# Kernel tuning notes

Hardware: AMD Instinct MI355X
Metric: run time of the kernel (lower is better)

Reference implementation:

```python
import jax, jax.numpy as jnp
import numpy as np

B, N, FIN, FOUT, OPD = 2048, 64, 96, 128, 48
EPS = 1e-5      # nn.LayerNorm default eps
SLOPE = 0.01    # F.leaky_relu default negative_slope (used in GAT forward)


def setup_inputs() -> dict:
    key = jax.random.key(0)
    ks = jax.random.split(key, 12)
    stdv = 1.0 / np.sqrt(FOUT)
    h = jax.random.normal(ks[0], (B, N, FIN), jnp.float32)
    # binary DAG-style adjacency (float mask, as used multiplicatively in torch)
    adj = (jax.random.uniform(ks[1], (B, N, N)) < 0.3).astype(jnp.float32)
    op_emb = jax.random.normal(ks[2], (B, N, OPD), jnp.float32)
    # DenseGraphFlow params (uniform(-stdv, stdv) per reset_parameters)
    W = jax.random.uniform(ks[3], (FIN, FOUT), jnp.float32, -stdv, stdv)
    b = jax.random.uniform(ks[4], (FOUT,), jnp.float32, -stdv, stdv)
    Wop_d = jax.random.normal(ks[5], (OPD, FOUT), jnp.float32) * 0.05
    bop_d = jnp.zeros((FOUT,), jnp.float32)
    # GraphAttentionLayer params
    Wk = jax.random.normal(ks[6], (FIN, FOUT), jnp.float32) * 0.05
    a_w = jax.random.normal(ks[7], (FOUT,), jnp.float32) * 0.05
    Wop_g = jax.random.normal(ks[8], (OPD, FOUT), jnp.float32) * 0.05
    bop_g = jnp.zeros((FOUT,), jnp.float32)
    gamma = jnp.ones((FOUT,), jnp.float32)
    beta = jnp.zeros((FOUT,), jnp.float32)
    return dict(h=h, adj=adj, op_emb=op_emb, W=W, b=b, Wop_d=Wop_d, bop_d=bop_d,
                Wk=Wk, a_w=a_w, Wop_g=Wop_g, bop_g=bop_g, gamma=gamma, beta=beta)


def reference(h, adj, op_emb, W, b, Wop_d, bop_d, Wk, a_w, Wop_g, bop_g, gamma, beta):
    # ---- DenseGraphFlow (residual=True, opattention=True) ----
    support = jnp.einsum('bnf,fo->bno', h, W)                       # [B,N,FOUT]
    gate_d = jax.nn.sigmoid(op_emb @ Wop_d + bop_d)                 # [B,N,FOUT]
    dense = gate_d * jnp.einsum('bij,bjo->bio', adj, support) + support + b

    # ---- GraphAttentionLayer (unique_attn_proj=False -> Wq=Wv=Wk) ----
    Whk = jnp.einsum('bnf,fo->bno', h, Wk)                          # [B,N,FOUT]
    # torch builds a_input[b,i,j,m] = Whk[b,j,m] * Whk[b,i,m], then projects with
    # a (Linear FOUT->1). Exactly equivalent factored form (no [B,N,N,F] tensor):
    scores = jnp.einsum('bim,bjm->bij', Whk * a_w, Whk)             # [B,N,N]
    alpha = jnp.where(scores >= 0, scores, SLOPE * scores) * adj    # leaky_relu then adj mask
    attn = jax.nn.softmax(alpha, axis=-1)                           # softmax over j (torch dim=-2 of [b,i,j,1])
    hp = jnp.einsum('bij,bjo->bio', attn, Whk)                      # aggregate values
    gate_g = jax.nn.sigmoid(op_emb @ Wop_g + bop_g)
    hp = gate_g * hp
    # LayerNorm over last dim
    mu = jnp.mean(hp, axis=-1, keepdims=True)
    var = jnp.var(hp, axis=-1, keepdims=True)
    hp = (hp - mu) / jnp.sqrt(var + EPS) * gamma + beta

    # ---- ensemble combine ----
    return (dense + hp) / 2
```

## Files before the change

### kernel.cpp

```cpp
#include <hip/hip_runtime.h>

#define NB 2048
#define NN 64
#define KFIN 96
#define KFOUT 128
#define KOPD 48

typedef __attribute__((ext_vector_type(8))) short bf8;
typedef __attribute__((ext_vector_type(4))) float f32x4;
typedef __attribute__((ext_vector_type(4))) unsigned short us4;
typedef __attribute__((ext_vector_type(2))) __bf16 bfx2;

__device__ __forceinline__ unsigned short f2bf(float f) {
  __bf16 h = (__bf16)f;
  return __builtin_bit_cast(unsigned short, h);
}
__device__ __forceinline__ float bf2f(unsigned short s) {
  unsigned int u = ((unsigned int)s) << 16;
  return __builtin_bit_cast(float, u);
}
__device__ __forceinline__ us4 pack4(float a, float b, float c, float d) {
  us4 q; q.x = f2bf(a); q.y = f2bf(b); q.z = f2bf(c); q.w = f2bf(d); return q;
}
__device__ __forceinline__ bf8 pk8(float4 a, float4 b) {
  bf8 r;
  r[0] = (short)f2bf(a.x); r[1] = (short)f2bf(a.y); r[2] = (short)f2bf(a.z); r[3] = (short)f2bf(a.w);
  r[4] = (short)f2bf(b.x); r[5] = (short)f2bf(b.y); r[6] = (short)f2bf(b.z); r[7] = (short)f2bf(b.w);
  return r;
}
__device__ __forceinline__ unsigned int pk2(float lo, float hi) {
  bfx2 v; v[0] = (__bf16)lo; v[1] = (__bf16)hi;
  return __builtin_bit_cast(unsigned int, v);
}
__device__ __forceinline__ float unpk(unsigned int p, int hi) {
  return bf2f((unsigned short)(hi ? (p >> 16) : (p & 0xffffu)));
}
__device__ __forceinline__ float sigm(float x) {
  return __builtin_amdgcn_rcpf(1.f + __expf(-x));
}

__global__ void prep_weights(const float* __restrict__ W, const float* __restrict__ Wk,
                             const float* __restrict__ Wd, const float* __restrict__ Wg,
                             unsigned short* __restrict__ ws) {
  int idx = blockIdx.x * 256 + threadIdx.x;
  if (idx >= 40960) return;
  float v;
  if (idx < 24576) {
    int r  = (idx < 12288) ? idx : idx - 12288;
    const float* M = (idx < 12288) ? W : Wk;
    int nb = r / 1536, rem = r % 1536;
    int kb = rem / 512, rem2 = rem % 512;
    int l = rem2 >> 3, e = rem2 & 7;
    int o = nb * 16 + (l & 15);
    int k = kb * 32 + (l >> 4) * 8 + e;
    v = M[k * 128 + o];
  } else {
    int r  = (idx < 32768) ? idx - 24576 : idx - 32768;
    const float* M = (idx < 32768) ? Wd : Wg;
    int nb = r / 1024, rem = r % 1024;
    int kb = rem / 512, rem2 = rem % 512;
    int l = rem2 >> 3, e = rem2 & 7;
    int o = nb * 16 + (l & 15);
    int k = kb * 32 + (l >> 4) * 8 + e;
    v = (k < 48) ? M[k * 128 + o] : 0.f;
  }
  ws[idx] = f2bf(v);
}

#define LD1 68
#define LD2 132
#define LDA 68
__global__ __launch_bounds__(256, 5) void gin_fused(
    const float* __restrict__ hg, const float* __restrict__ adjg,
    const float* __restrict__ opeg, const float* __restrict__ bvec,
    const float* __restrict__ bopd, const float* __restrict__ bopg,
    const float* __restrict__ awv, const float* __restrict__ gmv,
    const float* __restrict__ btv, const unsigned short* __restrict__ ws,
    float* __restrict__ out) {
  __shared__ __align__(16) char smem[26112];
  unsigned short* buf1   = (unsigned short*)smem;
  unsigned short* attn_s = (unsigned short*)(smem + 17408);

  const int t  = threadIdx.x;
  const int b  = blockIdx.x;
  const int w  = t >> 6;
  const int l  = t & 63;
  const int lr = l & 15;
  const int lg = l >> 4;
  const int kcol = 8 * lg;
  const int arow = w * 16 + lr;
  const int rowb = w * 16 + lg * 4;

  const float* hrow = hg   + (size_t)b * (NN * KFIN) + arow * KFIN;
  const float* orow = opeg + (size_t)b * (NN * KOPD) + arow * KOPD;
  float* outp = out + (size_t)b * (NN * KFOUT);

  const unsigned short* WT  = ws;
  const unsigned short* WkT = ws + 12288;
  const unsigned short* WdT = ws + 24576;
  const unsigned short* WgT = ws + 32768;
  f32x4 zz = {0.f, 0.f, 0.f, 0.f};

  bf8 oa[2], ha[3];
  {
    float4 p0 = *(const float4*)(orow + kcol);
    float4 p1 = *(const float4*)(orow + kcol + 4);
    oa[0] = pk8(p0, p1);
    if (lg < 2) {
      float4 q0 = *(const float4*)(orow + 32 + kcol);
      float4 q1 = *(const float4*)(orow + 32 + kcol + 4);
      oa[1] = pk8(q0, q1);
    } else {
      bf8 z = {0, 0, 0, 0, 0, 0, 0, 0};
      oa[1] = z;
    }
  }
  #pragma unroll
  for (int kb = 0; kb < 3; ++kb) {
    float4 p0 = *(const float4*)(hrow + kb * 32 + kcol);
    float4 p1 = *(const float4*)(hrow + kb * 32 + kcol + 4);
    ha[kb] = pk8(p0, p1);
  }

  unsigned int gdp[8][2];
  {
    f32x4 gd[8] = {zz, zz, zz, zz, zz, zz, zz, zz};
    #pragma unroll
    for (int kb = 0; kb < 2; ++kb) {
      #pragma unroll
      for (int nb = 0; nb < 8; ++nb) {
        bf8 bb = *(const bf8*)(WdT + (nb * 2 + kb) * 512 + l * 8);
        gd[nb] = __builtin_amdgcn_mfma_f32_16x16x32_bf16(oa[kb], bb, gd[nb], 0, 0, 0);
      }
    }
    #pragma unroll
    for (int nb = 0; nb < 8; ++nb) {
      float bo = bopd[nb * 16 + lr];
      gdp[nb][0] = pk2(sigm(gd[nb][0] + bo), sigm(gd[nb][1] + bo));
      gdp[nb][1] = pk2(sigm(gd[nb][2] + bo), sigm(gd[nb][3] + bo));
    }
  }

  f32x4 sacc[8] = {zz, zz, zz, zz, zz, zz, zz, zz};
  #pragma unroll
  for (int kb = 0; kb < 3; ++kb) {
    #pragma unroll
    for (int nb = 0; nb < 8; ++nb) {
      bf8 bb = *(const bf8*)(WT + (nb * 3 + kb) * 512 + l * 8);
      sacc[nb] = __builtin_amdgcn_mfma_f32_16x16x32_bf16(ha[kb], bb, sacc[nb], 0, 0, 0);
    }
  }
  #pragma unroll
  for (int nb = 0; nb < 8; ++nb)
    *(us4*)(buf1 + (nb * 16 + lr) * LD1 + w * 16 + lg * 4) =
        pack4(sacc[nb][0], sacc[nb][1], sacc[nb][2], sacc[nb][3]);
  __syncthreads();

  unsigned int dnp[8][2];
  {
    const float* ajr = adjg + (size_t)b * (NN * NN) + arow * NN;
    bf8 aa[2];
    #pragma unroll
    for (int kb = 0; kb < 2; ++kb) {
      float4 p0 = *(const float4*)(ajr + kb * 32 + kcol);
      float4 p1 = *(const float4*)(ajr + kb * 32 + kcol + 4);
      aa[kb] = pk8(p0, p1);
    }
    #pragma unroll
    for (int nb = 0; nb < 8; ++nb) {
      f32x4 dacc = zz;
      #pragma unroll
      for (int kb = 0; kb < 2; ++kb) {
        bf8 bb = *(const bf8*)(buf1 + (nb * 16 + lr) * LD1 + kb * 32 + kcol);
        dacc = __builtin_amdgcn_mfma_f32_16x16x32_bf16(aa[kb], bb, dacc, 0, 0, 0);
      }
      float bc = bvec[nb * 16 + lr];
      float d0 = unpk(gdp[nb][0], 0) * dacc[0] + sacc[nb][0] + bc;
      float d1 = unpk(gdp[nb][0], 1) * dacc[1] + sacc[nb][1] + bc;
      float d2 = unpk(gdp[nb][1], 0) * dacc[2] + sacc[nb][2] + bc;
      float d3 = unpk(gdp[nb][1], 1) * dacc[3] + sacc[nb][3] + bc;
      dnp[nb][0] = pk2(d0, d1); dnp[nb][1] = pk2(d2, d3);
    }
  }

  f32x4 wacc[8] = {zz, zz, zz, zz, zz, zz, zz, zz};
  #pragma unroll
  for (int kb = 0; kb < 3; ++kb) {
    #pragma unroll
    for (int nb = 0; nb < 8; ++nb) {
      bf8 bb = *(const bf8*)(WkT + (nb * 3 + kb) * 512 + l * 8);
      wacc[nb] = __builtin_amdgcn_mfma_f32_16x16x32_bf16(ha[kb], bb, wacc[nb], 0, 0, 0);
    }
  }
  __syncthreads();

  #pragma unroll
  for (int nb = 0; nb < 8; ++nb) {
    int o = nb * 16 + lr;
    #pragma unroll
    for (int r = 0; r < 4; ++r)
      buf1[(w * 16 + lg * 4 + r) * LD2 + o] = f2bf(wacc[nb][r]);
  }

  unsigned int ggp[8][2];
  {
    f32x4 gg[8] = {zz, zz, zz, zz, zz, zz, zz, zz};
    #pragma unroll
    for (int kb = 0; kb < 2; ++kb) {
      #pragma unroll
      for (int nb = 0; nb < 8; ++nb) {
        bf8 bb = *(const bf8*)(WgT + (nb * 2 + kb) * 512 + l * 8);
        gg[nb] = __builtin_amdgcn_mfma_f32_16x16x32_bf16(oa[kb], bb, gg[nb], 0, 0, 0);
      }
    }
    #pragma unroll
    for (int nb = 0; nb < 8; ++nb) {
      float bo = bopg[nb * 16 + lr];
      ggp[nb][0] = pk2(sigm(gg[nb][0] + bo), sigm(gg[nb][1] + bo));
      ggp[nb][1] = pk2(sigm(gg[nb][2] + bo), sigm(gg[nb][3] + bo));
    }
  }

  float msk[4][4];
  #pragma unroll
  for (int jb = 0; jb < 4; ++jb)
    #pragma unroll
    for (int r = 0; r < 4; ++r)
      msk[jb][r] = adjg[(size_t)b * (NN * NN) + (rowb + r) * NN + jb * 16 + lr];

  __syncthreads();

  f32x4 sc[4] = {zz, zz, zz, zz};
  #pragma unroll
  for (int kb = 0; kb < 4; ++kb) {
    bf8 ar = *(const bf8*)(buf1 + arow * LD2 + kb * 32 + kcol);
    const float4* ap = (const float4*)(awv + kb * 32 + kcol);
    float4 a0 = ap[0], a1 = ap[1];
    bf8 a;
    a[0] = (short)f2bf(bf2f((unsigned short)ar[0]) * a0.x);
    a[1] = (short)f2bf(bf2f((unsigned short)ar[1]) * a0.y);
    a[2] = (short)f2bf(bf2f((unsigned short)ar[2]) * a0.z);
    a[3] = (short)f2bf(bf2f((unsigned short)ar[3]) * a0.w);
    a[4] = (short)f2bf(bf2f((unsigned short)ar[4]) * a1.x);
    a[5] = (short)f2bf(bf2f((unsigned short)ar[5]) * a1.y);
    a[6] = (short)f2bf(bf2f((unsigned short)ar[6]) * a1.z);
    a[7] = (short)f2bf(bf2f((unsigned short)ar[7]) * a1.w);
    #pragma unroll
    for (int jb = 0; jb < 4; ++jb) {
      bf8 bb = *(const bf8*)(buf1 + (jb * 16 + lr) * LD2 + kb * 32 + kcol);
      sc[jb] = __builtin_amdgcn_mfma_f32_16x16x32_bf16(a, bb, sc[jb], 0, 0, 0);
    }
  }

  float al[4][4];
  #pragma unroll
  for (int jb = 0; jb < 4; ++jb)
    #pragma unroll
    for (int r = 0; r < 4; ++r) {
      float s = sc[jb][r];
      al[jb][r] = (s >= 0.f ? s : 0.01f * s) * msk[jb][r];
    }
  #pragma unroll
  for (int r = 0; r < 4; ++r) {
    float m = fmaxf(fmaxf(al[0][r], al[1][r]), fmaxf(al[2][r], al[3][r]));
    m = fmaxf(m, __shfl_xor(m, 1));
    m = fmaxf(m, __shfl_xor(m, 2));
    m = fmaxf(m, __shfl_xor(m, 4));
    m = fmaxf(m, __shfl_xor(m, 8));
    float s0 = 0.f;
    #pragma unroll
    for (int jb = 0; jb < 4; ++jb) { float p = __expf(al[jb][r] - m); al[jb][r] = p; s0 += p; }
    s0 += __shfl_xor(s0, 1);
    s0 += __shfl_xor(s0, 2);
    s0 += __shfl_xor(s0, 4);
    s0 += __shfl_xor(s0, 8);
    float inv = __builtin_amdgcn_rcpf(s0);
    #pragma unroll
    for (int jb = 0; jb < 4; ++jb) al[jb][r] *= inv;
  }

  #pragma unroll
  for (int jb = 0; jb < 4; ++jb)
    #pragma unroll
    for (int r = 0; r < 4; ++r)
      attn_s[(rowb + r) * LDA + jb * 16 + lr] = f2bf(al[jb][r]);

  f32x4 hpacc[8] = {zz, zz, zz, zz, zz, zz, zz, zz};
  #pragma unroll
  for (int kb = 0; kb < 2; ++kb) {
    bf8 a = *(const bf8*)(attn_s + arow * LDA + kb * 32 + kcol);
    #pragma unroll
    for (int nb = 0; nb < 8; ++nb) {
      const unsigned short* gp = buf1 + (kb * 32 + 8 * lg) * LD2 + nb * 16 + lr;
      bf8 bb;
      #pragma unroll
      for (int e = 0; e < 8; ++e) bb[e] = (short)gp[e * LD2];
      hpacc[nb] = __builtin_amdgcn_mfma_f32_16x16x32_bf16(a, bb, hpacc[nb], 0, 0, 0);
    }
  }

  float gam[8], bet[8];
  #pragma unroll
  for (int nb = 0; nb < 8; ++nb) { gam[nb] = gmv[nb * 16 + lr]; bet[nb] = btv[nb * 16 + lr]; }
  #pragma unroll
  for (int r = 0; r < 4; ++r) {
    float hv[8]; float su = 0.f, sq = 0.f;
    #pragma unroll
    for (int nb = 0; nb < 8; ++nb) {
      float v = unpk(ggp[nb][r >> 1], r & 1) * hpacc[nb][r];
      hv[nb] = v; su += v; sq += v * v;
    }
    su += __shfl_xor(su, 1); su += __shfl_xor(su, 2);
    su += __shfl_xor(su, 4); su += __shfl_xor(su, 8);
    sq += __shfl_xor(sq, 1); sq += __shfl_xor(sq, 2);
    sq += __shfl_xor(sq, 4); sq += __shfl_xor(sq, 8);
    float mean = su * (1.f / 128.f);
    float var  = sq * (1.f / 128.f) - mean * mean;
    float rinv = rsqrtf(var + 1e-5f);
    int row = rowb + r;
    #pragma unroll
    for (int nb = 0; nb < 8; ++nb) {
      float hn = (hv[nb] - mean) * rinv * gam[nb] + bet[nb];
      float dv = unpk(dnp[nb][r >> 1], r & 1);
      outp[row * 128 + nb * 16 + lr] = (dv + hn) * 0.5f;
    }
  }
}

extern "C" void kernel_launch(void* const* d_in, const int* in_sizes, int n_in,
                              void* d_out, int out_size, void* d_ws, size_t ws_size,
                              hipStream_t stream) {
  const float* h     = (const float*)d_in[0];
  const float* adj   = (const float*)d_in[1];
  const float* ope   = (const float*)d_in[2];
  const float* W     = (const float*)d_in[3];
  const float* bvec  = (const float*)d_in[4];
  const float* Wopd  = (const float*)d_in[5];
  const float* bopd  = (const float*)d_in[6];
  const float* Wk    = (const float*)d_in[7];
  const float* a_w   = (const float*)d_in[8];
  const float* Wopg  = (const float*)d_in[9];
  const float* bopg  = (const float*)d_in[10];
  const float* gamma = (const float*)d_in[11];
  const float* beta  = (const float*)d_in[12];
  float* out = (float*)d_out;
  unsigned short* ws = (unsigned short*)d_ws;

  prep_weights<<<dim3(160), dim3(256), 0, stream>>>(W, Wk, Wopd, Wopg, ws);
  gin_fused<<<dim3(NB), dim3(256), 0, stream>>>(h, adj, ope, bvec, bopd, bopg,
                                                a_w, gamma, beta, ws, out);
}
```

Baseline: 121.4 us.

## Split output columns across two waves per row block with cross-wave LayerNorm

Moves to 512 threads per block, with each pair of waves sharing a 16-row block and each wave computing half of the 128 output columns. This halves per-thread accumulator registers and adds parallelism per graph. A small shared buffer exchanges LayerNorm partial sums between the paired waves, which adds one extra barrier. Support values are now kept bf16-packed, and the attention buffer becomes per-wave with a new padding. The score and softmax work is now duplicated across the two waves of each pair.

```diff
diff --git a/kernel.cpp b/kernel.cpp
--- a/kernel.cpp
+++ b/kernel.cpp
@@ -69,27 +69,31 @@
 
 #define LD1 68
 #define LD2 132
-#define LDA 68
-__global__ __launch_bounds__(256, 5) void gin_fused(
+#define LDA 72
+__global__ __launch_bounds__(512, 6) void gin_fused(
     const float* __restrict__ hg, const float* __restrict__ adjg,
     const float* __restrict__ opeg, const float* __restrict__ bvec,
     const float* __restrict__ bopd, const float* __restrict__ bopg,
     const float* __restrict__ awv, const float* __restrict__ gmv,
     const float* __restrict__ btv, const unsigned short* __restrict__ ws,
     float* __restrict__ out) {
-  __shared__ __align__(16) char smem[26112];
-  unsigned short* buf1   = (unsigned short*)smem;
-  unsigned short* attn_s = (unsigned short*)(smem + 17408);
-
-  const int t  = threadIdx.x;
-  const int b  = blockIdx.x;
-  const int w  = t >> 6;
-  const int l  = t & 63;
-  const int lr = l & 15;
-  const int lg = l >> 4;
+  __shared__ __align__(16) char smem[36864];
+  unsigned short* buf1  = (unsigned short*)smem;
+  unsigned short* attnb = (unsigned short*)(smem + 17408);
+  float2*         lnbuf = (float2*)(smem + 35840);
+
+  const int t    = threadIdx.x;
+  const int b    = blockIdx.x;
+  const int wave = t >> 6;
+  const int wr   = wave >> 1;
+  const int wc   = wave & 1;
+  const int l    = t & 63;
+  const int lr   = l & 15;
+  const int lg   = l >> 4;
   const int kcol = 8 * lg;
-  const int arow = w * 16 + lr;
-  const int rowb = w * 16 + lg * 4;
+  const int arow = wr * 16 + lr;
+  const int rowb = wr * 16 + lg * 4;
+  const int cb   = wc * 64;
 
   const float* hrow = hg   + (size_t)b * (NN * KFIN) + arow * KFIN;
   const float* orow = opeg + (size_t)b * (NN * KOPD) + arow * KOPD;
@@ -122,41 +126,47 @@
     ha[kb] = pk8(p0, p1);
   }
 
-  unsigned int gdp[8][2];
-  {
-    f32x4 gd[8] = {zz, zz, zz, zz, zz, zz, zz, zz};
+  unsigned int gdp[4][2];
+  {
+    f32x4 gd[4] = {zz, zz, zz, zz};
     #pragma unroll
     for (int kb = 0; kb < 2; ++kb) {
       #pragma unroll
-      for (int nb = 0; nb < 8; ++nb) {
-        bf8 bb = *(const bf8*)(WdT + (nb * 2 + kb) * 512 + l * 8);
+      for (int nb = 0; nb < 4; ++nb) {
+        bf8 bb = *(const bf8*)(WdT + ((wc * 4 + nb) * 2 + kb) * 512 + l * 8);
         gd[nb] = __builtin_amdgcn_mfma_f32_16x16x32_bf16(oa[kb], bb, gd[nb], 0, 0, 0);
       }
     }
     #pragma unroll
-    for (int nb = 0; nb < 8; ++nb) {
-      float bo = bopd[nb * 16 + lr];
+    for (int nb = 0; nb < 4; ++nb) {
+      float bo = bopd[cb + nb * 16 + lr];
       gdp[nb][0] = pk2(sigm(gd[nb][0] + bo), sigm(gd[nb][1] + bo));
       gdp[nb][1] = pk2(sigm(gd[nb][2] + bo), sigm(gd[nb][3] + bo));
     }
   }
 
-  f32x4 sacc[8] = {zz, zz, zz, zz, zz, zz, zz, zz};
-  #pragma unroll
-  for (int kb = 0; kb < 3; ++kb) {
-    #pragma unroll
-    for (int nb = 0; nb < 8; ++nb) {
-      bf8 bb = *(const bf8*)(WT + (nb * 3 + kb) * 512 + l * 8);
-      sacc[nb] = __builtin_amdgcn_mfma_f32_16x16x32_bf16(ha[kb], bb, sacc[nb], 0, 0, 0);
-    }
-  }
-  #pragma unroll
-  for (int nb = 0; nb < 8; ++nb)
-    *(us4*)(buf1 + (nb * 16 + lr) * LD1 + w * 16 + lg * 4) =
-        pack4(sacc[nb][0], sacc[nb][1], sacc[nb][2], sacc[nb][3]);
+  unsigned int sap[4][2];
+  {
+    f32x4 sacc[4] = {zz, zz, zz, zz};
+    #pragma unroll
+    for (int kb = 0; kb < 3; ++kb) {
+      #pragma unroll
+      for (int nb = 0; nb < 4; ++nb) {
+        bf8 bb = *(const bf8*)(WT + ((wc * 4 + nb) * 3 + kb) * 512 + l * 8);
+        sacc[nb] = __builtin_amdgcn_mfma_f32_16x16x32_bf16(ha[kb], bb, sacc[nb], 0, 0, 0);
+      }
+    }
+    #pragma unroll
+    for (int nb = 0; nb < 4; ++nb) {
+      *(us4*)(buf1 + (cb + nb * 16 + lr) * LD1 + wr * 16 + lg * 4) =
+          pack4(sacc[nb][0], sacc[nb][1], sacc[nb][2], sacc[nb][3]);
+      sap[nb][0] = pk2(sacc[nb][0], sacc[nb][1]);
+      sap[nb][1] = pk2(sacc[nb][2], sacc[nb][3]);
+    }
+  }
   __syncthreads();
 
-  unsigned int dnp[8][2];
+  unsigned int dnp[4][2];
   {
     const float* ajr = adjg + (size_t)b * (NN * NN) + arow * NN;
     bf8 aa[2];
@@ -167,55 +177,55 @@
       aa[kb] = pk8(p0, p1);
     }
     #pragma unroll
-    for (int nb = 0; nb < 8; ++nb) {
+    for (int nb = 0; nb < 4; ++nb) {
       f32x4 dacc = zz;
       #pragma unroll
       for (int kb = 0; kb < 2; ++kb) {
-        bf8 bb = *(const bf8*)(buf1 + (nb * 16 + lr) * LD1 + kb * 32 + kcol);
+        bf8 bb = *(const bf8*)(buf1 + (cb + nb * 16 + lr) * LD1 + kb * 32 + kcol);
         dacc = __builtin_amdgcn_mfma_f32_16x16x32_bf16(aa[kb], bb, dacc, 0, 0, 0);
       }
-      float bc = bvec[nb * 16 + lr];
-      float d0 = unpk(gdp[nb][0], 0) * dacc[0] + sacc[nb][0] + bc;
-      float d1 = unpk(gdp[nb][0], 1) * dacc[1] + sacc[nb][1] + bc;
-      float d2 = unpk(gdp[nb][1], 0) * dacc[2] + sacc[nb][2] + bc;
-      float d3 = unpk(gdp[nb][1], 1) * dacc[3] + sacc[nb][3] + bc;
+      float bc = bvec[cb + nb * 16 + lr];
+      float d0 = unpk(gdp[nb][0], 0) * dacc[0] + unpk(sap[nb][0], 0) + bc;
+      float d1 = unpk(gdp[nb][0], 1) * dacc[1] + unpk(sap[nb][0], 1) + bc;
+      float d2 = unpk(gdp[nb][1], 0) * dacc[2] + unpk(sap[nb][1], 0) + bc;
+      float d3 = unpk(gdp[nb][1], 1) * dacc[3] + unpk(sap[nb][1], 1) + bc;
       dnp[nb][0] = pk2(d0, d1); dnp[nb][1] = pk2(d2, d3);
     }
   }
 
-  f32x4 wacc[8] = {zz, zz, zz, zz, zz, zz, zz, zz};
+  f32x4 wacc[4] = {zz, zz, zz, zz};
   #pragma unroll
   for (int kb = 0; kb < 3; ++kb) {
     #pragma unroll
-    for (int nb = 0; nb < 8; ++nb) {
-      bf8 bb = *(const bf8*)(WkT + (nb * 3 + kb) * 512 + l * 8);
+    for (int nb = 0; nb < 4; ++nb) {
+      bf8 bb = *(const bf8*)(WkT + ((wc * 4 + nb) * 3 + kb) * 512 + l * 8);
       wacc[nb] = __builtin_amdgcn_mfma_f32_16x16x32_bf16(ha[kb], bb, wacc[nb], 0, 0, 0);
     }
   }
   __syncthreads();
 
   #pragma unroll
-  for (int nb = 0; nb < 8; ++nb) {
-    int o = nb * 16 + lr;
+  for (int nb = 0; nb < 4; ++nb) {
+    int o = cb + nb * 16 + lr;
     #pragma unroll
     for (int r = 0; r < 4; ++r)
-      buf1[(w * 16 + lg * 4 + r) * LD2 + o] = f2bf(wacc[nb][r]);
-  }
-
-  unsigned int ggp[8][2];
-  {
-    f32x4 gg[8] = {zz, zz, zz, zz, zz, zz, zz, zz};
+      buf1[(wr * 16 + lg * 4 + r) * LD2 + o] = f2bf(wacc[nb][r]);
+  }
+
+  unsigned int ggp[4][2];
+  {
+    f32x4 gg[4] = {zz, zz, zz, zz};
     #pragma unroll
     for (int kb = 0; kb < 2; ++kb) {
       #pragma unroll
-      for (int nb = 0; nb < 8; ++nb) {
-        bf8 bb = *(const bf8*)(WgT + (nb * 2 + kb) * 512 + l * 8);
+      for (int nb = 0; nb < 4; ++nb) {
+        bf8 bb = *(const bf8*)(WgT + ((wc * 4 + nb) * 2 + kb) * 512 + l * 8);
         gg[nb] = __builtin_amdgcn_mfma_f32_16x16x32_bf16(oa[kb], bb, gg[nb], 0, 0, 0);
       }
     }
     #pragma unroll
-    for (int nb = 0; nb < 8; ++nb) {
-      float bo = bopg[nb * 16 + lr];
+    for (int nb = 0; nb < 4; ++nb) {
+      float bo = bopg[cb + nb * 16 + lr];
       ggp[nb][0] = pk2(sigm(gg[nb][0] + bo), sigm(gg[nb][1] + bo));
       ggp[nb][1] = pk2(sigm(gg[nb][2] + bo), sigm(gg[nb][3] + bo));
     }
@@ -279,19 +289,20 @@
     for (int jb = 0; jb < 4; ++jb) al[jb][r] *= inv;
   }
 
+  unsigned short* attnw = attnb + wave * (16 * LDA);
   #pragma unroll
   for (int jb = 0; jb < 4; ++jb)
     #pragma unroll
     for (int r = 0; r < 4; ++r)
-      attn_s[(rowb + r) * LDA + jb * 16 + lr] = f2bf(al[jb][r]);
-
-  f32x4 hpacc[8] = {zz, zz, zz, zz, zz, zz, zz, zz};
+      attnw[(lg * 4 + r) * LDA + jb * 16 + lr] = f2bf(al[jb][r]);
+
+  f32x4 hpacc[4] = {zz, zz, zz, zz};
   #pragma unroll
   for (int kb = 0; kb < 2; ++kb) {
-    bf8 a = *(const bf8*)(attn_s + arow * LDA + kb * 32 + kcol);
-    #pragma unroll
-    for (int nb = 0; nb < 8; ++nb) {
-      const unsigned short* gp = buf1 + (kb * 32 + 8 * lg) * LD2 + nb * 16 + lr;
+    bf8 a = *(const bf8*)(attnw + lr * LDA + kb * 32 + kcol);
+    #pragma unroll
+    for (int nb = 0; nb < 4; ++nb) {
+      const unsigned short* gp = buf1 + (kb * 32 + 8 * lg) * LD2 + cb + nb * 16 + lr;
       bf8 bb;
       #pragma unroll
       for (int e = 0; e < 8; ++e) bb[e] = (short)gp[e * LD2];
@@ -299,30 +310,47 @@
     }
   }
 
-  float gam[8], bet[8];
-  #pragma unroll
-  for (int nb = 0; nb < 8; ++nb) { gam[nb] = gmv[nb * 16 + lr]; bet[nb] = btv[nb * 16 + lr]; }
+  float hv[4][4], su4[4], sq4[4];
   #pragma unroll
   for (int r = 0; r < 4; ++r) {
-    float hv[8]; float su = 0.f, sq = 0.f;
-    #pragma unroll
-    for (int nb = 0; nb < 8; ++nb) {
+    float su = 0.f, sq = 0.f;
+    #pragma unroll
+    for (int nb = 0; nb < 4; ++nb) {
       float v = unpk(ggp[nb][r >> 1], r & 1) * hpacc[nb][r];
-      hv[nb] = v; su += v; sq += v * v;
+      hv[r][nb] = v; su += v; sq += v * v;
     }
     su += __shfl_xor(su, 1); su += __shfl_xor(su, 2);
     su += __shfl_xor(su, 4); su += __shfl_xor(su, 8);
     sq += __shfl_xor(sq, 1); sq += __shfl_xor(sq, 2);
     sq += __shfl_xor(sq, 4); sq += __shfl_xor(sq, 8);
+    su4[r] = su; sq4[r] = sq;
+    if (lr == 0) {
+      float2 p; p.x = su; p.y = sq;
+      lnbuf[(rowb + r) * 2 + wc] = p;
+    }
+  }
+  __syncthreads();
+
+  float gam[4], bet[4];
+  #pragma unroll
+  for (int nb = 0; nb < 4; ++nb) {
+    gam[nb] = gmv[cb + nb * 16 + lr];
+    bet[nb] = btv[cb + nb * 16 + lr];
+  }
+  #pragma unroll
+  for (int r = 0; r < 4; ++r) {
+    float2 o2 = lnbuf[(rowb + r) * 2 + (wc ^ 1)];
+    float su = su4[r] + o2.x;
+    float sq = sq4[r] + o2.y;
     float mean = su * (1.f / 128.f);
     float var  = sq * (1.f / 128.f) - mean * mean;
     float rinv = rsqrtf(var + 1e-5f);
     int row = rowb + r;
     #pragma unroll
-    for (int nb = 0; nb < 8; ++nb) {
-      float hn = (hv[nb] - mean) * rinv * gam[nb] + bet[nb];
+    for (int nb = 0; nb < 4; ++nb) {
+      float hn = (hv[r][nb] - mean) * rinv * gam[nb] + bet[nb];
       float dv = unpk(dnp[nb][r >> 1], r & 1);
-      outp[row * 128 + nb * 16 + lr] = (dv + hn) * 0.5f;
+      outp[row * 128 + cb + nb * 16 + lr] = (dv + hn) * 0.5f;
     }
   }
 }
@@ -347,6 +375,6 @@
   unsigned short* ws = (unsigned short*)d_ws;
 
   prep_weights<<<dim3(160), dim3(256), 0, stream>>>(W, Wk, Wopd, Wopg, ws);
-  gin_fused<<<dim3(NB), dim3(256), 0, stream>>>(h, adj, ope, bvec, bopd, bopg,
+  gin_fused<<<dim3(NB), dim3(512), 0, stream>>>(h, adj, ope, bvec, bopd, bopg,
                                                 a_w, gamma, beta, ws, out);
 }
```

After: 184.7 us. +52.2%, slower.
